# Optimization experiments

Hardware: AMD Instinct MI355X
Metric: run time of the kernel (lower is better)

Reference implementation:

```python
import jax, jax.numpy as jnp
import numpy as np

B, NCAMS = 1, 6
C_FEAT = 64                     # fusion_feat_in_dim
H, W = 88, 160                  # per-camera feature map size at fusion level
VOX_SIZE = (100, 100, 20)       # (x_dim, y_dim, z_dim) voxel counts
VOX_STR = (-50.0, -50.0, -15.0)
VOX_UNIT = (1.0, 1.0, 1.5)
N_VOX = VOX_SIZE[0] * VOX_SIZE[1] * VOX_SIZE[2]
EPS = 1e-8
V_PRE = 64                      # voxel_pre_dim[0]


def make_voxel_pts(dtype):
    # [B, 4, N]; homogeneous (x, y, z, 1) points, layout [z, y, x] flattened
    xs = jnp.linspace(VOX_STR[0], VOX_STR[0] + VOX_UNIT[0] * (VOX_SIZE[0] - 1), VOX_SIZE[0], dtype=dtype)
    ys = jnp.linspace(VOX_STR[1], VOX_STR[1] + VOX_UNIT[1] * (VOX_SIZE[1] - 1), VOX_SIZE[1], dtype=dtype)
    zs = jnp.linspace(VOX_STR[2], VOX_STR[2] + VOX_UNIT[2] * (VOX_SIZE[2] - 1), VOX_SIZE[2], dtype=dtype)
    zdim, ydim, xdim = VOX_SIZE[2], VOX_SIZE[1], VOX_SIZE[0]
    gx = jnp.broadcast_to(xs[None, None, :], (zdim, ydim, xdim)).reshape(-1)
    gy = jnp.broadcast_to(ys[None, :, None], (zdim, ydim, xdim)).reshape(-1)
    gz = jnp.broadcast_to(zs[:, None, None], (zdim, ydim, xdim)).reshape(-1)
    pts = jnp.stack([gx, gy, gz, jnp.ones_like(gx)], axis=0)  # [4, N]
    return jnp.broadcast_to(pts[None], (B, 4, N_VOX))


def _gather(imgf, iy, ix, Wd):
    # imgf: [BN, C, H*W]; iy/ix: [BN, N] int32 -> [BN, C, N]
    lin = iy * Wd + ix
    return jnp.take_along_axis(imgf, lin[:, None, :], axis=2)


def bilinear_sample(img, gx, gy):
    # grid_sample(mode='bilinear', padding_mode='zeros', align_corners=True)
    BN, C, Hd, Wd = img.shape
    x = (gx + 1.0) * 0.5 * (Wd - 1)
    y = (gy + 1.0) * 0.5 * (Hd - 1)
    x0 = jnp.floor(x); y0 = jnp.floor(y)
    wx1 = x - x0; wx0 = 1.0 - wx1
    wy1 = y - y0; wy0 = 1.0 - wy1
    imgf = img.reshape(BN, C, Hd * Wd)
    out = jnp.zeros((BN, C, gx.shape[1]), dtype=img.dtype)
    for xi, wxi in ((x0, wx0), (x0 + 1.0, wx1)):
        for yi, wyi in ((y0, wy0), (y0 + 1.0, wy1)):
            valid = (xi >= 0) & (xi <= Wd - 1) & (yi >= 0) & (yi <= Hd - 1)
            ii = jnp.clip(xi, 0, Wd - 1).astype(jnp.int32)
            jj = jnp.clip(yi, 0, Hd - 1).astype(jnp.int32)
            w = (wxi * wyi * valid.astype(img.dtype))[:, None, :]
            out = out + _gather(imgf, jj, ii, Wd) * w
    return out


def nearest_sample(img, gx, gy):
    # grid_sample(mode='nearest', padding_mode='zeros', align_corners=True)
    BN, C, Hd, Wd = img.shape
    x = (gx + 1.0) * 0.5 * (Wd - 1)
    y = (gy + 1.0) * 0.5 * (Hd - 1)
    xi = jnp.round(x); yi = jnp.round(y)
    valid = (xi >= 0) & (xi <= Wd - 1) & (yi >= 0) & (yi <= Hd - 1)
    ii = jnp.clip(xi, 0, Wd - 1).astype(jnp.int32)
    jj = jnp.clip(yi, 0, Hd - 1).astype(jnp.int32)
    imgf = img.reshape(BN, C, Hd * Wd)
    return _gather(imgf, jj, ii, Wd) * valid[:, None, :].astype(img.dtype)


def setup_inputs() -> dict:
    key = jax.random.key(0)
    ks = jax.random.split(key, 8)
    return {
        'multi_img_feat': jax.random.normal(ks[0], (B, NCAMS, C_FEAT, H, W), jnp.float32),
        'mask': jax.random.uniform(ks[1], (B, NCAMS, 1, H, W), jnp.float32),
        'K': jax.random.normal(ks[2], (B, NCAMS, 4, 4), jnp.float32),
        'extrinsics': jax.random.normal(ks[3], (B, NCAMS, 4, 4), jnp.float32),
        'w_no': jax.random.normal(ks[4], (V_PRE, C_FEAT + 1), jnp.float32) * 0.05,
        'b_no': jax.random.normal(ks[5], (V_PRE,), jnp.float32) * 0.05,
        'w_o': jax.random.normal(ks[6], (V_PRE, 2 * (C_FEAT + 1)), jnp.float32) * 0.05,
        'b_o': jax.random.normal(ks[7], (V_PRE,), jnp.float32) * 0.05,
    }


def reference(multi_img_feat, mask, K, extrinsics, w_no, b_no, w_o, b_o):
    Bb, NC, C, Hd, Wd = multi_img_feat.shape
    dt = multi_img_feat.dtype
    vpts = make_voxel_pts(dt)                                          # [B,4,N]
    vpts_c = jnp.broadcast_to(vpts[:, None], (Bb, NC, 4, N_VOX)).reshape(Bb * NC, 4, N_VOX)
    feats = multi_img_feat.reshape(Bb * NC, C, Hd, Wd)
    masks = mask.reshape(Bb * NC, 1, Hd, Wd)                           # interp to (H,W) is identity (same size, align_corners)
    ext = extrinsics.reshape(Bb * NC, 4, 4)[:, :3, :]
    K3 = K.reshape(Bb * NC, 4, 4)[:, :3, :3]

    v_local = jnp.einsum('bij,bjn->bin', ext, vpts_c)                  # [BN,3,N]
    cam_pts = jnp.einsum('bij,bjn->bin', K3, v_local)
    pix = cam_pts[:, :2] / (cam_pts[:, 2:3] + EPS)
    pix = jnp.where(jnp.all(jnp.isfinite(pix)), pix, jnp.clip(pix, -Wd * 2.0, Wd * 2.0))
    gx = (pix[:, 0] / (Wd - 1) - 0.5) * 2.0                            # [BN,N] normalized coords
    gy = (pix[:, 1] / (Hd - 1) - 0.5) * 2.0

    feat_w = bilinear_sample(feats, gx, gy)                            # [BN,C,N]
    m_occ = nearest_sample(masks, gx, gy) > 0.5                        # [BN,1,N]
    m_depth = v_local[:, 2:3] > 0
    oob = (gx > 1) | (gx < -1) | (gy > 1) | (gy < -1)
    valid = (m_occ & m_depth & (~oob)[:, None, :]).astype(dt)          # [BN,1,N]

    feat_w = jnp.concatenate([feat_w, v_local[:, 2:3] / VOX_SIZE[0]], axis=1) * valid  # [BN,C+1,N]

    feat_w = feat_w.reshape(Bb, NC, C + 1, N_VOX)
    valid = valid.reshape(Bb, NC, 1, N_VOX)
    count = valid.sum(axis=1)                                          # [B,1,N]

    # non-overlap branch: voxels seen by exactly one camera
    no_mask = (count == 1).astype(dt)
    vox_no = feat_w.sum(axis=1) * no_mask
    vox_no = jax.nn.elu(jnp.einsum('oc,bcn->bon', w_no, vox_no) + b_no[None, :, None]) * no_mask

    # overlap branch: cams {0,3,4} vs {1,2,5}
    o_mask = (count == 2).astype(dt)
    feat1 = feat_w[:, 0] + feat_w[:, 3] + feat_w[:, 4]
    feat2 = feat_w[:, 1] + feat_w[:, 2] + feat_w[:, 5]
    vox_o = jnp.concatenate([feat1, feat2], axis=1)                    # [B,2*(C+1),N]
    vox_o = jax.nn.elu(jnp.einsum('oc,bcn->bon', w_o, vox_o) + b_o[None, :, None]) * o_mask

    return vox_no + vox_o                                              # [B, V_PRE, N]
```

## Files before the change

kernel.cpp:

```cpp
#include <hip/hip_runtime.h>
#include <cmath>

#define NC 6
#define CF 64
#define HH 88
#define WW 160
#define NPIX 14080
#define NVOX 200000
#define VPRE 64
#define VB 512
#define NTH 512
#define NWV 8

typedef unsigned int u32;

#define FEATT_BYTES  (6u * 64u * 14080u * 4u)

__global__ __launch_bounds__(256) void transpose_feats(const float* __restrict__ in,
                                                       float* __restrict__ out) {
    __shared__ float tile[64 * 65];
    int blk = blockIdx.x;
    int c = blk / 220;
    int p0 = (blk - c * 220) * 64;
    int tid = threadIdx.x;
    int lane = tid & 63;
    int quad = tid >> 6;
    for (int r = quad; r < 64; r += 4)
        tile[r * 65 + lane] = in[(c * 64 + r) * NPIX + p0 + lane];
    __syncthreads();
    for (int r = quad; r < 64; r += 4)
        out[((c * NPIX) + p0 + r) * 64 + lane] = tile[lane * 65 + r];
}

__device__ __forceinline__ float elu1(float x) { return x > 0.0f ? x : expm1f(x); }

__device__ __forceinline__ float gather_bilin(const float* __restrict__ fsrc, int useT,
                                              int lane, int cam, float x, float y) {
    float x0f = floorf(x), y0f = floorf(y);
    float wx1 = x - x0f, wx0 = 1.0f - wx1;
    float wy1 = y - y0f, wy0 = 1.0f - wy1;
    float x1f = x0f + 1.0f, y1f = y0f + 1.0f;
    float bx0 = (x0f >= 0.0f && x0f <= 159.0f) ? 1.0f : 0.0f;
    float bx1 = (x1f >= 0.0f && x1f <= 159.0f) ? 1.0f : 0.0f;
    float by0 = (y0f >= 0.0f && y0f <= 87.0f) ? 1.0f : 0.0f;
    float by1 = (y1f >= 0.0f && y1f <= 87.0f) ? 1.0f : 0.0f;
    int ix0 = (int)fminf(fmaxf(x0f, 0.0f), 159.0f);
    int ix1 = (int)fminf(fmaxf(x1f, 0.0f), 159.0f);
    int iy0 = (int)fminf(fmaxf(y0f, 0.0f), 87.0f);
    int iy1 = (int)fminf(fmaxf(y1f, 0.0f), 87.0f);
    int A = useT ? 64 : 1;
    int Boff = useT ? (cam * NPIX * 64 + lane) : ((cam * 64 + lane) * NPIX);
    float v00 = fsrc[(iy0 * WW + ix0) * A + Boff];
    float v01 = fsrc[(iy1 * WW + ix0) * A + Boff];
    float v10 = fsrc[(iy0 * WW + ix1) * A + Boff];
    float v11 = fsrc[(iy1 * WW + ix1) * A + Boff];
    float fv;
    fv  = (wx0 * wy0 * bx0 * by0) * v00;
    fv += (wx0 * wy1 * bx0 * by1) * v01;
    fv += (wx1 * wy0 * bx1 * by0) * v10;
    fv += (wx1 * wy1 * bx1 * by1) * v11;
    return fv;
}

#define FMA8_STEP(W0,W1,W2,W3,W4,W5,W6,W7,CG,F0,F1,F2,F3) \
    a0 += W0[CG]*F0; a0 += W0[CG+1]*F1; a0 += W0[CG+2]*F2; a0 += W0[CG+3]*F3; \
    a1 += W1[CG]*F0; a1 += W1[CG+1]*F1; a1 += W1[CG+2]*F2; a1 += W1[CG+3]*F3; \
    a2 += W2[CG]*F0; a2 += W2[CG+1]*F1; a2 += W2[CG+2]*F2; a2 += W2[CG+3]*F3; \
    a3 += W3[CG]*F0; a3 += W3[CG+1]*F1; a3 += W3[CG+2]*F2; a3 += W3[CG+3]*F3; \
    a4 += W4[CG]*F0; a4 += W4[CG+1]*F1; a4 += W4[CG+2]*F2; a4 += W4[CG+3]*F3; \
    a5 += W5[CG]*F0; a5 += W5[CG+1]*F1; a5 += W5[CG+2]*F2; a5 += W5[CG+3]*F3; \
    a6 += W6[CG]*F0; a6 += W6[CG+1]*F1; a6 += W6[CG+2]*F2; a6 += W6[CG+3]*F3; \
    a7 += W7[CG]*F0; a7 += W7[CG+1]*F1; a7 += W7[CG+2]*F2; a7 += W7[CG+3]*F3;

__global__ __launch_bounds__(NTH) void vox_fused(
    const float* __restrict__ feats,
    const float* __restrict__ featT,
    const float* __restrict__ mask,
    const float* __restrict__ Kg,
    const float* __restrict__ ext,
    const float* __restrict__ wno,
    const float* __restrict__ bno,
    const float* __restrict__ wo,
    const float* __restrict__ bo,
    float* __restrict__ outp,
    int useT)
{
    __shared__ float s_ext[72];
    __shared__ float s_K[54];
    __shared__ float s_F[65 * 66];
    __shared__ __align__(16) float4 s_rec1[VB];
    __shared__ __align__(16) float4 s_rec2[2 * VB];
    __shared__ int s_vox[64];
    __shared__ int s_n1, s_n2;

    int tid = threadIdx.x;
    int lane = tid & 63;
    int wv = tid >> 6;
    int base = blockIdx.x * VB;
    int vlim = min(VB, NVOX - base);

    if (tid == 0) { s_n1 = 0; s_n2 = 0; }
    if (tid >= 64 && tid < 136) {
        int i = tid - 64;
        s_ext[i] = ext[(i / 12) * 16 + (i % 12)];
    }
    if (tid >= 192 && tid < 246) {
        int i = tid - 192; int cam = i / 9; int e = i - cam * 9;
        s_K[i] = Kg[cam * 16 + (e / 3) * 4 + (e % 3)];
    }

    {
        int ng4 = vlim >> 2;
        for (int i = tid; i < 64 * 128; i += NTH) {
            int r = i >> 7, cg = i & 127;
            if (cg < ng4)
                *(float4*)(outp + (size_t)r * NVOX + base + (cg << 2)) =
                    make_float4(0.f, 0.f, 0.f, 0.f);
        }
    }
    __syncthreads();

    if (tid < vlim) {
        #pragma clang fp contract(off)
        int n = base + tid;
        int xi = n % 100;
        int t = n / 100;
        int yi = t % 100;
        int zi = t / 100;
        float X = -50.0f + (float)xi;
        float Y = -50.0f + (float)yi;
        float Z = -15.0f + 1.5f * (float)zi;
        int cnt = 0, cam0 = 0, cam1 = 0;
        float ax = 0.f, ay = 0.f, az = 0.f, bx = 0.f, by = 0.f, bz = 0.f;
        #pragma unroll
        for (int cam = 0; cam < NC; ++cam) {
            const float* E = s_ext + cam * 12;
            const float* Kk = s_K + cam * 9;
            float vl0 = E[0]*X + E[1]*Y + E[2]*Z + E[3];
            float vl1 = E[4]*X + E[5]*Y + E[6]*Z + E[7];
            float vl2 = E[8]*X + E[9]*Y + E[10]*Z + E[11];
            float c0 = Kk[0]*vl0 + Kk[1]*vl1 + Kk[2]*vl2;
            float c1 = Kk[3]*vl0 + Kk[4]*vl1 + Kk[5]*vl2;
            float c2 = Kk[6]*vl0 + Kk[7]*vl1 + Kk[8]*vl2;
            float pz = c2 + 1e-8f;
            float px = c0 / pz;
            float py = c1 / pz;
            float gx = (px / 159.0f - 0.5f) * 2.0f;
            float gy = (py / 87.0f - 0.5f) * 2.0f;
            float x = ((gx + 1.0f) * 0.5f) * 159.0f;
            float y = ((gy + 1.0f) * 0.5f) * 87.0f;
            float xr = rintf(x), yr = rintf(y);
            bool nv = (xr >= 0.0f) && (xr <= 159.0f) && (yr >= 0.0f) && (yr <= 87.0f);
            float mval = 0.0f;
            if (nv) mval = mask[(cam * HH + (int)yr) * WW + (int)xr];
            bool ok = (mval > 0.5f) && (vl2 > 0.0f) &&
                      !((gx > 1.0f) || (gx < -1.0f) || (gy > 1.0f) || (gy < -1.0f));
            if (ok) {
                if (cnt == 0) { ax = x; ay = y; az = vl2; cam0 = cam; }
                else if (cnt == 1) { bx = x; by = y; bz = vl2; cam1 = cam; }
                ++cnt;
            }
        }
        if (cnt == 1) {
            int s = atomicAdd(&s_n1, 1);
            s_rec1[s] = make_float4(ax, ay, az, __int_as_float((n << 3) | cam0));
        } else if (cnt == 2) {
            int s = atomicAdd(&s_n2, 1);
            s_rec2[2 * s + 0] = make_float4(ax, ay, az, __int_as_float((n << 3) | cam0));
            s_rec2[2 * s + 1] = make_float4(bx, by, bz, __int_as_float((n << 3) | cam1));
        }
    }
    __syncthreads();

    int n1 = s_n1, n2 = s_n2;
    const float* fsrc = useT ? featT : feats;
    int wvu = __builtin_amdgcn_readfirstlane(wv);
    int obase = wvu * 8;
    const float* w0n = wno + (obase + 0) * 65;
    const float* w1n = wno + (obase + 1) * 65;
    const float* w2n = wno + (obase + 2) * 65;
    const float* w3n = wno + (obase + 3) * 65;
    const float* w4n = wno + (obase + 4) * 65;
    const float* w5n = wno + (obase + 5) * 65;
    const float* w6n = wno + (obase + 6) * 65;
    const float* w7n = wno + (obase + 7) * 65;
    const float* w0o = wo + (obase + 0) * 130;
    const float* w1o = wo + (obase + 1) * 130;
    const float* w2o = wo + (obase + 2) * 130;
    const float* w3o = wo + (obase + 3) * 130;
    const float* w4o = wo + (obase + 4) * 130;
    const float* w5o = wo + (obase + 5) * 130;
    const float* w6o = wo + (obase + 6) * 130;
    const float* w7o = wo + (obase + 7) * 130;

    for (int t0 = 0; t0 < n1; t0 += 64) {
        int tl = min(64, n1 - t0);
        for (int e = wv; e < tl; e += NWV) {
            float4 r = s_rec1[t0 + e];
            int meta = __float_as_int(r.w);
            int cam = meta & 7;
            float fv = gather_bilin(fsrc, useT, lane, cam, r.x, r.y);
            s_F[lane * 66 + e] = fv;
            if (lane == 0) { s_F[64 * 66 + e] = r.z / 100.0f; s_vox[e] = meta >> 3; }
        }
        __syncthreads();
        float a0 = bno[obase + 0], a1 = bno[obase + 1], a2 = bno[obase + 2], a3 = bno[obase + 3];
        float a4 = bno[obase + 4], a5 = bno[obase + 5], a6 = bno[obase + 6], a7 = bno[obase + 7];
        for (int cg = 0; cg < 64; cg += 4) {
            float f0 = s_F[(cg + 0) * 66 + lane];
            float f1 = s_F[(cg + 1) * 66 + lane];
            float f2 = s_F[(cg + 2) * 66 + lane];
            float f3 = s_F[(cg + 3) * 66 + lane];
            FMA8_STEP(w0n, w1n, w2n, w3n, w4n, w5n, w6n, w7n, cg, f0, f1, f2, f3)
        }
        float fd = s_F[64 * 66 + lane];
        a0 += w0n[64] * fd; a1 += w1n[64] * fd; a2 += w2n[64] * fd; a3 += w3n[64] * fd;
        a4 += w4n[64] * fd; a5 += w5n[64] * fd; a6 += w6n[64] * fd; a7 += w7n[64] * fd;
        if (lane < tl) {
            size_t col = (size_t)s_vox[lane];
            outp[(size_t)(obase + 0) * NVOX + col] = elu1(a0);
            outp[(size_t)(obase + 1) * NVOX + col] = elu1(a1);
            outp[(size_t)(obase + 2) * NVOX + col] = elu1(a2);
            outp[(size_t)(obase + 3) * NVOX + col] = elu1(a3);
            outp[(size_t)(obase + 4) * NVOX + col] = elu1(a4);
            outp[(size_t)(obase + 5) * NVOX + col] = elu1(a5);
            outp[(size_t)(obase + 6) * NVOX + col] = elu1(a6);
            outp[(size_t)(obase + 7) * NVOX + col] = elu1(a7);
        }
        __syncthreads();
    }

    for (int t0 = 0; t0 < n2; t0 += 64) {
        int tl = min(64, n2 - t0);
        for (int e = wv; e < tl; e += NWV) {
            float4 r0 = s_rec2[2 * (t0 + e) + 0];
            float4 r1 = s_rec2[2 * (t0 + e) + 1];
            int m0 = __float_as_int(r0.w), m1 = __float_as_int(r1.w);
            int ca = m0 & 7, cb = m1 & 7;
            float fg = 0.0f, dd = 0.0f;
            if (!(ca == 1 || ca == 2 || ca == 5)) {
                fg += gather_bilin(fsrc, useT, lane, ca, r0.x, r0.y);
                dd += r0.z / 100.0f;
            }
            if (!(cb == 1 || cb == 2 || cb == 5)) {
                fg += gather_bilin(fsrc, useT, lane, cb, r1.x, r1.y);
                dd += r1.z / 100.0f;
            }
            s_F[lane * 66 + e] = fg;
            if (lane == 0) { s_F[64 * 66 + e] = dd; s_vox[e] = m0 >> 3; }
        }
        __syncthreads();
        float a0 = bo[obase + 0], a1 = bo[obase + 1], a2 = bo[obase + 2], a3 = bo[obase + 3];
        float a4 = bo[obase + 4], a5 = bo[obase + 5], a6 = bo[obase + 6], a7 = bo[obase + 7];
        for (int cg = 0; cg < 64; cg += 4) {
            float f0 = s_F[(cg + 0) * 66 + lane];
            float f1 = s_F[(cg + 1) * 66 + lane];
            float f2 = s_F[(cg + 2) * 66 + lane];
            float f3 = s_F[(cg + 3) * 66 + lane];
            FMA8_STEP(w0o, w1o, w2o, w3o, w4o, w5o, w6o, w7o, cg, f0, f1, f2, f3)
        }
        {
            float fd = s_F[64 * 66 + lane];
            a0 += w0o[64] * fd; a1 += w1o[64] * fd; a2 += w2o[64] * fd; a3 += w3o[64] * fd;
            a4 += w4o[64] * fd; a5 += w5o[64] * fd; a6 += w6o[64] * fd; a7 += w7o[64] * fd;
        }
        __syncthreads();
        for (int e = wv; e < tl; e += NWV) {
            float4 r0 = s_rec2[2 * (t0 + e) + 0];
            float4 r1 = s_rec2[2 * (t0 + e) + 1];
            int m0 = __float_as_int(r0.w), m1 = __float_as_int(r1.w);
            int ca = m0 & 7, cb = m1 & 7;
            float fg = 0.0f, dd = 0.0f;
            if (ca == 1 || ca == 2 || ca == 5) {
                fg += gather_bilin(fsrc, useT, lane, ca, r0.x, r0.y);
                dd += r0.z / 100.0f;
            }
            if (cb == 1 || cb == 2 || cb == 5) {
                fg += gather_bilin(fsrc, useT, lane, cb, r1.x, r1.y);
                dd += r1.z / 100.0f;
            }
            s_F[lane * 66 + e] = fg;
            if (lane == 0) s_F[64 * 66 + e] = dd;
        }
        __syncthreads();
        for (int cg = 0; cg < 64; cg += 4) {
            float f0 = s_F[(cg + 0) * 66 + lane];
            float f1 = s_F[(cg + 1) * 66 + lane];
            float f2 = s_F[(cg + 2) * 66 + lane];
            float f3 = s_F[(cg + 3) * 66 + lane];
            int cgo = cg + 65;
            FMA8_STEP(w0o, w1o, w2o, w3o, w4o, w5o, w6o, w7o, cgo, f0, f1, f2, f3)
        }
        {
            float fd = s_F[64 * 66 + lane];
            a0 += w0o[129] * fd; a1 += w1o[129] * fd; a2 += w2o[129] * fd; a3 += w3o[129] * fd;
            a4 += w4o[129] * fd; a5 += w5o[129] * fd; a6 += w6o[129] * fd; a7 += w7o[129] * fd;
        }
        if (lane < tl) {
            size_t col = (size_t)s_vox[lane];
            outp[(size_t)(obase + 0) * NVOX + col] = elu1(a0);
            outp[(size_t)(obase + 1) * NVOX + col] = elu1(a1);
            outp[(size_t)(obase + 2) * NVOX + col] = elu1(a2);
            outp[(size_t)(obase + 3) * NVOX + col] = elu1(a3);
            outp[(size_t)(obase + 4) * NVOX + col] = elu1(a4);
            outp[(size_t)(obase + 5) * NVOX + col] = elu1(a5);
            outp[(size_t)(obase + 6) * NVOX + col] = elu1(a6);
            outp[(size_t)(obase + 7) * NVOX + col] = elu1(a7);
        }
        __syncthreads();
    }
}

extern "C" void kernel_launch(void* const* d_in, const int* in_sizes, int n_in,
                              void* d_out, int out_size, void* d_ws, size_t ws_size,
                              hipStream_t stream) {
    const float* feats = (const float*)d_in[0];
    const float* mask  = (const float*)d_in[1];
    const float* Kg    = (const float*)d_in[2];
    const float* ext   = (const float*)d_in[3];
    const float* wno   = (const float*)d_in[4];
    const float* bno   = (const float*)d_in[5];
    const float* wo    = (const float*)d_in[6];
    const float* bo    = (const float*)d_in[7];
    float* outp = (float*)d_out;
    float* featT = (float*)d_ws;

    int useT = (ws_size >= (size_t)FEATT_BYTES) ? 1 : 0;
    if (useT) {
        transpose_feats<<<NC * 220, 256, 0, stream>>>(feats, featT);
    }
    int nblk = (NVOX + VB - 1) / VB;
    vox_fused<<<nblk, NTH, 0, stream>>>(feats, featT, mask, Kg, ext,
                                        wno, bno, wo, bo, outp, useT);
}
```

Before: 177.8 us.

## Shrink voxel blocks to 128 with 4 waves each computing 16 output channels

The voxel block drops from 512 to 128 voxels and threads per block from 512 to 256. Each of the 4 wavefronts now computes 16 output channels instead of 8, so the same staged shared-memory feature tile is reused for twice as many channels. Smaller blocks mean more blocks across the 200000 voxels, and compaction tiles are more often full, which should cut partial-tile waste and improve load balance. The cost is more accumulator and weight registers per thread, which may lower occupancy, plus more per-block setup and zero-fill overhead. The gather work for each 64-voxel tile is split across fewer waves.

```diff
diff --git a/kernel.cpp b/kernel.cpp
--- a/kernel.cpp
+++ b/kernel.cpp
@@ -8,9 +8,9 @@
 #define NPIX 14080
 #define NVOX 200000
 #define VPRE 64
-#define VB 512
-#define NTH 512
-#define NWV 8
+#define VB 128
+#define NTH 256
+#define NWV 4
 
 typedef unsigned int u32;
 
@@ -62,15 +62,47 @@
     return fv;
 }
 
-#define FMA8_STEP(W0,W1,W2,W3,W4,W5,W6,W7,CG,F0,F1,F2,F3) \
-    a0 += W0[CG]*F0; a0 += W0[CG+1]*F1; a0 += W0[CG+2]*F2; a0 += W0[CG+3]*F3; \
-    a1 += W1[CG]*F0; a1 += W1[CG+1]*F1; a1 += W1[CG+2]*F2; a1 += W1[CG+3]*F3; \
-    a2 += W2[CG]*F0; a2 += W2[CG+1]*F1; a2 += W2[CG+2]*F2; a2 += W2[CG+3]*F3; \
-    a3 += W3[CG]*F0; a3 += W3[CG+1]*F1; a3 += W3[CG+2]*F2; a3 += W3[CG+3]*F3; \
-    a4 += W4[CG]*F0; a4 += W4[CG+1]*F1; a4 += W4[CG+2]*F2; a4 += W4[CG+3]*F3; \
-    a5 += W5[CG]*F0; a5 += W5[CG+1]*F1; a5 += W5[CG+2]*F2; a5 += W5[CG+3]*F3; \
-    a6 += W6[CG]*F0; a6 += W6[CG+1]*F1; a6 += W6[CG+2]*F2; a6 += W6[CG+3]*F3; \
-    a7 += W7[CG]*F0; a7 += W7[CG+1]*F1; a7 += W7[CG+2]*F2; a7 += W7[CG+3]*F3;
+#define FMA16_STEP(WB,RS,CG,F0,F1,F2,F3) \
+    a0  += WB[ 0*RS+CG]*F0; a0  += WB[ 0*RS+CG+1]*F1; a0  += WB[ 0*RS+CG+2]*F2; a0  += WB[ 0*RS+CG+3]*F3; \
+    a1  += WB[ 1*RS+CG]*F0; a1  += WB[ 1*RS+CG+1]*F1; a1  += WB[ 1*RS+CG+2]*F2; a1  += WB[ 1*RS+CG+3]*F3; \
+    a2  += WB[ 2*RS+CG]*F0; a2  += WB[ 2*RS+CG+1]*F1; a2  += WB[ 2*RS+CG+2]*F2; a2  += WB[ 2*RS+CG+3]*F3; \
+    a3  += WB[ 3*RS+CG]*F0; a3  += WB[ 3*RS+CG+1]*F1; a3  += WB[ 3*RS+CG+2]*F2; a3  += WB[ 3*RS+CG+3]*F3; \
+    a4  += WB[ 4*RS+CG]*F0; a4  += WB[ 4*RS+CG+1]*F1; a4  += WB[ 4*RS+CG+2]*F2; a4  += WB[ 4*RS+CG+3]*F3; \
+    a5  += WB[ 5*RS+CG]*F0; a5  += WB[ 5*RS+CG+1]*F1; a5  += WB[ 5*RS+CG+2]*F2; a5  += WB[ 5*RS+CG+3]*F3; \
+    a6  += WB[ 6*RS+CG]*F0; a6  += WB[ 6*RS+CG+1]*F1; a6  += WB[ 6*RS+CG+2]*F2; a6  += WB[ 6*RS+CG+3]*F3; \
+    a7  += WB[ 7*RS+CG]*F0; a7  += WB[ 7*RS+CG+1]*F1; a7  += WB[ 7*RS+CG+2]*F2; a7  += WB[ 7*RS+CG+3]*F3; \
+    a8  += WB[ 8*RS+CG]*F0; a8  += WB[ 8*RS+CG+1]*F1; a8  += WB[ 8*RS+CG+2]*F2; a8  += WB[ 8*RS+CG+3]*F3; \
+    a9  += WB[ 9*RS+CG]*F0; a9  += WB[ 9*RS+CG+1]*F1; a9  += WB[ 9*RS+CG+2]*F2; a9  += WB[ 9*RS+CG+3]*F3; \
+    a10 += WB[10*RS+CG]*F0; a10 += WB[10*RS+CG+1]*F1; a10 += WB[10*RS+CG+2]*F2; a10 += WB[10*RS+CG+3]*F3; \
+    a11 += WB[11*RS+CG]*F0; a11 += WB[11*RS+CG+1]*F1; a11 += WB[11*RS+CG+2]*F2; a11 += WB[11*RS+CG+3]*F3; \
+    a12 += WB[12*RS+CG]*F0; a12 += WB[12*RS+CG+1]*F1; a12 += WB[12*RS+CG+2]*F2; a12 += WB[12*RS+CG+3]*F3; \
+    a13 += WB[13*RS+CG]*F0; a13 += WB[13*RS+CG+1]*F1; a13 += WB[13*RS+CG+2]*F2; a13 += WB[13*RS+CG+3]*F3; \
+    a14 += WB[14*RS+CG]*F0; a14 += WB[14*RS+CG+1]*F1; a14 += WB[14*RS+CG+2]*F2; a14 += WB[14*RS+CG+3]*F3; \
+    a15 += WB[15*RS+CG]*F0; a15 += WB[15*RS+CG+1]*F1; a15 += WB[15*RS+CG+2]*F2; a15 += WB[15*RS+CG+3]*F3;
+
+#define FMA16_DEPTH(WB,RS,CI,FD) \
+    a0  += WB[ 0*RS+CI]*FD; a1  += WB[ 1*RS+CI]*FD; a2  += WB[ 2*RS+CI]*FD; a3  += WB[ 3*RS+CI]*FD; \
+    a4  += WB[ 4*RS+CI]*FD; a5  += WB[ 5*RS+CI]*FD; a6  += WB[ 6*RS+CI]*FD; a7  += WB[ 7*RS+CI]*FD; \
+    a8  += WB[ 8*RS+CI]*FD; a9  += WB[ 9*RS+CI]*FD; a10 += WB[10*RS+CI]*FD; a11 += WB[11*RS+CI]*FD; \
+    a12 += WB[12*RS+CI]*FD; a13 += WB[13*RS+CI]*FD; a14 += WB[14*RS+CI]*FD; a15 += WB[15*RS+CI]*FD;
+
+#define STORE16(COL) \
+    outp[(size_t)(obase + 0)  * NVOX + COL] = elu1(a0);  \
+    outp[(size_t)(obase + 1)  * NVOX + COL] = elu1(a1);  \
+    outp[(size_t)(obase + 2)  * NVOX + COL] = elu1(a2);  \
+    outp[(size_t)(obase + 3)  * NVOX + COL] = elu1(a3);  \
+    outp[(size_t)(obase + 4)  * NVOX + COL] = elu1(a4);  \
+    outp[(size_t)(obase + 5)  * NVOX + COL] = elu1(a5);  \
+    outp[(size_t)(obase + 6)  * NVOX + COL] = elu1(a6);  \
+    outp[(size_t)(obase + 7)  * NVOX + COL] = elu1(a7);  \
+    outp[(size_t)(obase + 8)  * NVOX + COL] = elu1(a8);  \
+    outp[(size_t)(obase + 9)  * NVOX + COL] = elu1(a9);  \
+    outp[(size_t)(obase + 10) * NVOX + COL] = elu1(a10); \
+    outp[(size_t)(obase + 11) * NVOX + COL] = elu1(a11); \
+    outp[(size_t)(obase + 12) * NVOX + COL] = elu1(a12); \
+    outp[(size_t)(obase + 13) * NVOX + COL] = elu1(a13); \
+    outp[(size_t)(obase + 14) * NVOX + COL] = elu1(a14); \
+    outp[(size_t)(obase + 15) * NVOX + COL] = elu1(a15);
 
 __global__ __launch_bounds__(NTH) void vox_fused(
     const float* __restrict__ feats,
@@ -111,8 +143,8 @@
 
     {
         int ng4 = vlim >> 2;
-        for (int i = tid; i < 64 * 128; i += NTH) {
-            int r = i >> 7, cg = i & 127;
+        for (int i = tid; i < 64 * (VB / 4); i += NTH) {
+            int r = i >> 5, cg = i & ((VB / 4) - 1);
             if (cg < ng4)
                 *(float4*)(outp + (size_t)r * NVOX + base + (cg << 2)) =
                     make_float4(0.f, 0.f, 0.f, 0.f);
@@ -175,23 +207,9 @@
     int n1 = s_n1, n2 = s_n2;
     const float* fsrc = useT ? featT : feats;
     int wvu = __builtin_amdgcn_readfirstlane(wv);
-    int obase = wvu * 8;
-    const float* w0n = wno + (obase + 0) * 65;
-    const float* w1n = wno + (obase + 1) * 65;
-    const float* w2n = wno + (obase + 2) * 65;
-    const float* w3n = wno + (obase + 3) * 65;
-    const float* w4n = wno + (obase + 4) * 65;
-    const float* w5n = wno + (obase + 5) * 65;
-    const float* w6n = wno + (obase + 6) * 65;
-    const float* w7n = wno + (obase + 7) * 65;
-    const float* w0o = wo + (obase + 0) * 130;
-    const float* w1o = wo + (obase + 1) * 130;
-    const float* w2o = wo + (obase + 2) * 130;
-    const float* w3o = wo + (obase + 3) * 130;
-    const float* w4o = wo + (obase + 4) * 130;
-    const float* w5o = wo + (obase + 5) * 130;
-    const float* w6o = wo + (obase + 6) * 130;
-    const float* w7o = wo + (obase + 7) * 130;
+    int obase = wvu * 16;
+    const float* wbn = wno + obase * 65;
+    const float* wbo = wo + obase * 130;
 
     for (int t0 = 0; t0 < n1; t0 += 64) {
         int tl = min(64, n1 - t0);
@@ -204,28 +222,24 @@
             if (lane == 0) { s_F[64 * 66 + e] = r.z / 100.0f; s_vox[e] = meta >> 3; }
         }
         __syncthreads();
-        float a0 = bno[obase + 0], a1 = bno[obase + 1], a2 = bno[obase + 2], a3 = bno[obase + 3];
-        float a4 = bno[obase + 4], a5 = bno[obase + 5], a6 = bno[obase + 6], a7 = bno[obase + 7];
+        float a0  = bno[obase + 0],  a1  = bno[obase + 1],  a2  = bno[obase + 2],  a3  = bno[obase + 3];
+        float a4  = bno[obase + 4],  a5  = bno[obase + 5],  a6  = bno[obase + 6],  a7  = bno[obase + 7];
+        float a8  = bno[obase + 8],  a9  = bno[obase + 9],  a10 = bno[obase + 10], a11 = bno[obase + 11];
+        float a12 = bno[obase + 12], a13 = bno[obase + 13], a14 = bno[obase + 14], a15 = bno[obase + 15];
         for (int cg = 0; cg < 64; cg += 4) {
             float f0 = s_F[(cg + 0) * 66 + lane];
             float f1 = s_F[(cg + 1) * 66 + lane];
             float f2 = s_F[(cg + 2) * 66 + lane];
             float f3 = s_F[(cg + 3) * 66 + lane];
-            FMA8_STEP(w0n, w1n, w2n, w3n, w4n, w5n, w6n, w7n, cg, f0, f1, f2, f3)
-        }
-        float fd = s_F[64 * 66 + lane];
-        a0 += w0n[64] * fd; a1 += w1n[64] * fd; a2 += w2n[64] * fd; a3 += w3n[64] * fd;
-        a4 += w4n[64] * fd; a5 += w5n[64] * fd; a6 += w6n[64] * fd; a7 += w7n[64] * fd;
+            FMA16_STEP(wbn, 65, cg, f0, f1, f2, f3)
+        }
+        {
+            float fd = s_F[64 * 66 + lane];
+            FMA16_DEPTH(wbn, 65, 64, fd)
+        }
         if (lane < tl) {
             size_t col = (size_t)s_vox[lane];
-            outp[(size_t)(obase + 0) * NVOX + col] = elu1(a0);
-            outp[(size_t)(obase + 1) * NVOX + col] = elu1(a1);
-            outp[(size_t)(obase + 2) * NVOX + col] = elu1(a2);
-            outp[(size_t)(obase + 3) * NVOX + col] = elu1(a3);
-            outp[(size_t)(obase + 4) * NVOX + col] = elu1(a4);
-            outp[(size_t)(obase + 5) * NVOX + col] = elu1(a5);
-            outp[(size_t)(obase + 6) * NVOX + col] = elu1(a6);
-            outp[(size_t)(obase + 7) * NVOX + col] = elu1(a7);
+            STORE16(col)
         }
         __syncthreads();
     }
@@ -250,19 +264,20 @@
             if (lane == 0) { s_F[64 * 66 + e] = dd; s_vox[e] = m0 >> 3; }
         }
         __syncthreads();
-        float a0 = bo[obase + 0], a1 = bo[obase + 1], a2 = bo[obase + 2], a3 = bo[obase + 3];
-        float a4 = bo[obase + 4], a5 = bo[obase + 5], a6 = bo[obase + 6], a7 = bo[obase + 7];
+        float a0  = bo[obase + 0],  a1  = bo[obase + 1],  a2  = bo[obase + 2],  a3  = bo[obase + 3];
+        float a4  = bo[obase + 4],  a5  = bo[obase + 5],  a6  = bo[obase + 6],  a7  = bo[obase + 7];
+        float a8  = bo[obase + 8],  a9  = bo[obase + 9],  a10 = bo[obase + 10], a11 = bo[obase + 11];
+        float a12 = bo[obase + 12], a13 = bo[obase + 13], a14 = bo[obase + 14], a15 = bo[obase + 15];
         for (int cg = 0; cg < 64; cg += 4) {
             float f0 = s_F[(cg + 0) * 66 + lane];
             float f1 = s_F[(cg + 1) * 66 + lane];
             float f2 = s_F[(cg + 2) * 66 + lane];
             float f3 = s_F[(cg + 3) * 66 + lane];
-            FMA8_STEP(w0o, w1o, w2o, w3o, w4o, w5o, w6o, w7o, cg, f0, f1, f2, f3)
+            FMA16_STEP(wbo, 130, cg, f0, f1, f2, f3)
         }
         {
             float fd = s_F[64 * 66 + lane];
-            a0 += w0o[64] * fd; a1 += w1o[64] * fd; a2 += w2o[64] * fd; a3 += w3o[64] * fd;
-            a4 += w4o[64] * fd; a5 += w5o[64] * fd; a6 += w6o[64] * fd; a7 += w7o[64] * fd;
+            FMA16_DEPTH(wbo, 130, 64, fd)
         }
         __syncthreads();
         for (int e = wv; e < tl; e += NWV) {
@@ -289,23 +304,15 @@
             float f2 = s_F[(cg + 2) * 66 + lane];
             float f3 = s_F[(cg + 3) * 66 + lane];
             int cgo = cg + 65;
-            FMA8_STEP(w0o, w1o, w2o, w3o, w4o, w5o, w6o, w7o, cgo, f0, f1, f2, f3)
+            FMA16_STEP(wbo, 130, cgo, f0, f1, f2, f3)
         }
         {
             float fd = s_F[64 * 66 + lane];
-            a0 += w0o[129] * fd; a1 += w1o[129] * fd; a2 += w2o[129] * fd; a3 += w3o[129] * fd;
-            a4 += w4o[129] * fd; a5 += w5o[129] * fd; a6 += w6o[129] * fd; a7 += w7o[129] * fd;
+            FMA16_DEPTH(wbo, 130, 129, fd)
         }
         if (lane < tl) {
             size_t col = (size_t)s_vox[lane];
-            outp[(size_t)(obase + 0) * NVOX + col] = elu1(a0);
-            outp[(size_t)(obase + 1) * NVOX + col] = elu1(a1);
-            outp[(size_t)(obase + 2) * NVOX + col] = elu1(a2);
-            outp[(size_t)(obase + 3) * NVOX + col] = elu1(a3);
-            outp[(size_t)(obase + 4) * NVOX + col] = elu1(a4);
-            outp[(size_t)(obase + 5) * NVOX + col] = elu1(a5);
-            outp[(size_t)(obase + 6) * NVOX + col] = elu1(a6);
-            outp[(size_t)(obase + 7) * NVOX + col] = elu1(a7);
+            STORE16(col)
         }
         __syncthreads();
     }
```

New measurement: 167.3 us. -5.9%, faster.
